# Kernel tuning notes

Measured on AMD Instinct MI355X. Metric: run time of the kernel, lower is better.

The kernel has to match this reference:

```python
import jax, jax.numpy as jnp
import numpy as np

N = 50000   # nodes
E = 800000  # edges
H = 3       # attention heads
IN_F = 128
HID = 128
NUM_CLASSES = 6
GAT_SLOPE = 0.2   # DGL GATConv internal leaky_relu slope
ACT_SLOPE = 0.01  # nn.LeakyReLU default


def setup_inputs() -> dict:
    key = jax.random.key(0)
    ks = jax.random.split(key, 24)
    s = 0.05
    inp = {
        "in_feat": jax.random.normal(ks[0], (N, IN_F), jnp.float32),
        "src": jax.random.randint(ks[1], (E,), 0, N, jnp.int32),
        "dst": jax.random.randint(ks[2], (E,), 0, N, jnp.int32),
        # GATConv 1: W (IN_F, H*HID), attn vectors (H, HID), bias (H*HID)
        "W1": jax.random.normal(ks[3], (IN_F, H * HID), jnp.float32) * s,
        "al1": jax.random.normal(ks[4], (H, HID), jnp.float32) * s,
        "ar1": jax.random.normal(ks[5], (H, HID), jnp.float32) * s,
        "b1": jnp.zeros((H * HID,), jnp.float32),
        # GATConv 2
        "W2": jax.random.normal(ks[6], (HID, H * HID), jnp.float32) * s,
        "al2": jax.random.normal(ks[7], (H, HID), jnp.float32) * s,
        "ar2": jax.random.normal(ks[8], (H, HID), jnp.float32) * s,
        "b2": jnp.zeros((H * HID,), jnp.float32),
    }
    # Dense MLP head lin1..lin4 (HID->HID) and lin5 (HID->NUM_CLASSES)
    for i in range(1, 5):
        inp[f"lw{i}"] = jax.random.normal(ks[8 + 2 * i], (HID, HID), jnp.float32) * s
        inp[f"lb{i}"] = jnp.zeros((HID,), jnp.float32)
    inp["lw5"] = jax.random.normal(ks[20], (HID, NUM_CLASSES), jnp.float32) * s
    inp["lb5"] = jnp.zeros((NUM_CLASSES,), jnp.float32)
    return inp


def gat_conv(x, src, dst, W, al, ar, b):
    # x: (N, F_in) -> out: (N, H, HID)
    h = (x @ W).reshape(N, H, HID)
    el = jnp.einsum('nhf,hf->nh', h, al)  # (N, H)
    er = jnp.einsum('nhf,hf->nh', h, ar)
    e = jax.nn.leaky_relu(el[src] + er[dst], GAT_SLOPE)  # (E, H)
    # edge softmax over incoming edges of each dst node
    m = jax.ops.segment_max(e, dst, num_segments=N)
    m = jnp.where(jnp.isfinite(m), m, 0.0)
    ex = jnp.exp(e - m[dst])
    denom = jax.ops.segment_sum(ex, dst, num_segments=N)
    alpha = ex / (denom[dst] + 1e-9)  # (E, H)
    out = jax.ops.segment_sum(alpha[:, :, None] * h[src], dst, num_segments=N)
    return out + b.reshape(1, H, HID)


def reference(in_feat, src, dst, W1, al1, ar1, b1, W2, al2, ar2, b2,
              lw1, lb1, lw2, lb2, lw3, lb3, lw4, lb4, lw5, lb5):
    act = lambda x: jax.nn.leaky_relu(x, ACT_SLOPE)
    h = act(gat_conv(in_feat, src, dst, W1, al1, ar1, b1)).mean(axis=1)
    h = act(gat_conv(h, src, dst, W2, al2, ar2, b2)).mean(axis=1)
    h = act(h @ lw1 + lb1)
    h = act(h @ lw2 + lb2)
    h = act(h @ lw3 + lb3)
    h = act(h @ lw4 + lb4)
    return h @ lw5 + lb5
```

## Files before the change

### kernel.cpp

```cpp
#include <hip/hip_runtime.h>
#include <hip/hip_bf16.h>


typedef __attribute__((ext_vector_type(8))) short short8;
typedef __attribute__((ext_vector_type(4))) float float4v;
typedef __attribute__((ext_vector_type(2))) float floatx2;

__device__ inline short f2bf(float x) {
    union { float f; unsigned u; } v; v.f = x;
    unsigned r = v.u + 0x7FFFu + ((v.u >> 16) & 1u);
    return (short)(r >> 16);
}
__device__ inline float bf2f(short b) {
    union { float f; unsigned u; } v;
    v.u = ((unsigned)(unsigned short)b) << 16;
    return v.f;
}
__device__ inline short8 zero8() { short8 z = {0,0,0,0,0,0,0,0}; return z; }

#if __has_builtin(__builtin_amdgcn_cvt_pk_fp8_f32)
__device__ inline unsigned short pk2fp8(float a, float b) {
    return (unsigned short)(__builtin_amdgcn_cvt_pk_fp8_f32(a, b, 0, false) & 0xFFFF);
}
#else
__device__ inline unsigned char f2fp8_1(float x) {
    union { float f; unsigned u; } v; v.f = x;
    unsigned s = (v.u >> 24) & 0x80u;
    unsigned au = v.u & 0x7FFFFFFFu;
    if (au >= 0x43E00000u) return (unsigned char)(s | 0x7E);
    if (au < 0x3C800000u) {
        union { float f; unsigned u; } a; a.u = au;
        int k = (int)(a.f * 512.0f + 0.5f);
        if (k > 7) return (unsigned char)(s | 0x08);
        return (unsigned char)(s | (unsigned)k);
    }
    unsigned r = au + 0x0007FFFFu + ((au >> 20) & 1u);
    unsigned e = (r >> 23) - 120u;
    unsigned m = (r >> 20) & 7u;
    if (e >= 15u && m >= 7u) { e = 15u; m = 6u; }
    return (unsigned char)(s | (e << 3) | m);
}
__device__ inline unsigned short pk2fp8(float a, float b) {
    return (unsigned short)f2fp8_1(a) | ((unsigned short)f2fp8_1(b) << 8);
}
#endif

#if __has_builtin(__builtin_amdgcn_cvt_pk_f32_fp8)
__device__ inline floatx2 unpk2fp8(unsigned short p) {
    return __builtin_amdgcn_cvt_pk_f32_fp8((int)p, false);
}
#else
__device__ inline float fp8_1_2f(unsigned char b) {
    unsigned s = b >> 7, e = (b >> 3) & 15u, m = b & 7u;
    float v = (e == 0) ? (float)m * 0.001953125f
                       : (float)(8u + m) * exp2f((float)((int)e - 10));
    return s ? -v : v;
}
__device__ inline floatx2 unpk2fp8(unsigned short p) {
    floatx2 r; r.x = fp8_1_2f((unsigned char)(p & 0xFF));
    r.y = fp8_1_2f((unsigned char)(p >> 8)); return r;
}
#endif

__device__ __forceinline__ void gl_lds16(const short* g, short* l) {
    __builtin_amdgcn_global_load_lds(
        (const __attribute__((address_space(1))) void*)g,
        (__attribute__((address_space(3))) void*)l,
        16, 0, 0);
}

#define SW(r) ((((r) >> 2) ^ (r)) & 3)

#define BM 128
#define BN 128
#define BK 32
#define MSTR 136
#define MROWS 64

__global__ void prep_kernel(
    const float* __restrict__ in_feat, short* __restrict__ P1h,
    short* __restrict__ P1l, int n4, int cb, int wb,
    const int* __restrict__ dst, int* __restrict__ cnt, int E,
    const float* __restrict__ w1, const float* __restrict__ w2,
    const float* __restrict__ m1, const float* __restrict__ m2,
    const float* __restrict__ m3, const float* __restrict__ m4,
    const float* __restrict__ w5,
    short* __restrict__ w1h, short* __restrict__ w1l,
    short* __restrict__ w2h, short* __restrict__ w2l,
    short* __restrict__ m1h, short* __restrict__ m1l,
    short* __restrict__ m2h, short* __restrict__ m2l,
    short* __restrict__ m3h, short* __restrict__ m3l,
    short* __restrict__ m4h, short* __restrict__ m4l,
    short* __restrict__ w5h, short* __restrict__ w5l)
{
    int blk = blockIdx.x;
    if (blk < cb) {
        int i = blk * 256 + threadIdx.x;
        if (i >= n4) return;
        float4 v = *(const float4*)(in_feat + (size_t)i * 4);
        float xs[4] = {v.x, v.y, v.z, v.w};
        short hs[4], ls[4];
        #pragma unroll
        for (int j = 0; j < 4; ++j) {
            hs[j] = f2bf(xs[j]);
            ls[j] = f2bf(xs[j] - bf2f(hs[j]));
        }
        *(uint2*)(P1h + (size_t)i * 4) = *(uint2*)hs;
        *(uint2*)(P1l + (size_t)i * 4) = *(uint2*)ls;
    } else if (blk < cb + wb) {
        int j = (blk - cb) * 256 + threadIdx.x;
        const float* src; short* th; short* tl; int Nc, base;
        if      (j < 49152)  { src = w1; th = w1h; tl = w1l; Nc = 384; base = 0; }
        else if (j < 98304)  { src = w2; th = w2h; tl = w2l; Nc = 384; base = 49152; }
        else if (j < 114688) { src = m1; th = m1h; tl = m1l; Nc = 128; base = 98304; }
        else if (j < 131072) { src = m2; th = m2h; tl = m2l; Nc = 128; base = 114688; }
        else if (j < 147456) { src = m3; th = m3h; tl = m3l; Nc = 128; base = 131072; }
        else if (j < 163840) { src = m4; th = m4h; tl = m4l; Nc = 128; base = 147456; }
        else if (j < 164608) { src = w5; th = w5h; tl = w5l; Nc = 6;   base = 163840; }
        else return;
        int i = j - base;
        int k = i / Nc, c = i - k * Nc;
        float v = src[i];
        short h = f2bf(v);
        th[(size_t)c * 128 + k] = h;
        tl[(size_t)c * 128 + k] = f2bf(v - bf2f(h));
    } else {
        int e = (blk - cb - wb) * 256 + threadIdx.x;
        if (e < E) atomicAdd(&cnt[dst[e]], 1);
    }
}

__global__ __launch_bounds__(256) void gemm_mfma(
    const short* __restrict__ Ahi, const short* __restrict__ Alo,
    const short* __restrict__ Bth, const short* __restrict__ Btl,
    const float* __restrict__ bias,
    float* __restrict__ Cf, short* __restrict__ Chi, short* __restrict__ Clo,
    unsigned char* __restrict__ Cf8,
    float* __restrict__ el, float* __restrict__ er,
    const float* __restrict__ al, const float* __restrict__ ar,
    int M, int Nc, int flags)
{
    __shared__ short Ah[BM * BK], Al_[BM * BK];
    __shared__ short Bh[BN * BK], Bl_[BN * BK];

    int tid = threadIdx.x, lane = tid & 63, wave = tid >> 6;
    int l15 = lane & 15, q = lane >> 4;
    int rowBase = blockIdx.y * BM, colBase = blockIdx.x * BN;

    float4v acc[2][8];
    #pragma unroll
    for (int mt = 0; mt < 2; ++mt)
        #pragma unroll
        for (int nt = 0; nt < 8; ++nt)
            acc[mt][nt] = (float4v){0.f, 0.f, 0.f, 0.f};

    for (int k0 = 0; k0 < 128; k0 += BK) {
        #pragma unroll
        for (int i = 0; i < 2; ++i) {
            int cid = tid + i * 256;
            int r = cid >> 2, sub = cid & 3;
            int gs = (sub ^ SW(r)) * 8;
            size_t ga = (size_t)(rowBase + r) * 128 + k0 + gs;
            size_t gb = (size_t)(colBase + r) * 128 + k0 + gs;
            int ld = cid * 8;
            gl_lds16(Ahi + ga, Ah  + ld);
            gl_lds16(Alo + ga, Al_ + ld);
            gl_lds16(Bth + gb, Bh  + ld);
            gl_lds16(Btl + gb, Bl_ + ld);
        }
        __syncthreads();

        short8 aH[2], aL2[2];
        #pragma unroll
        for (int mt = 0; mt < 2; ++mt) {
            int row = wave * 32 + mt * 16 + l15;
            int off = row * 32 + (q ^ SW(row)) * 8;
            aH[mt]  = *(short8*)&Ah[off];
            aL2[mt] = *(short8*)&Al_[off];
        }
        #pragma unroll
        for (int nt = 0; nt < 8; ++nt) {
            int row = nt * 16 + l15;
            int off = row * 32 + (q ^ SW(row)) * 8;
            short8 bH = *(short8*)&Bh[off];
            short8 bL = *(short8*)&Bl_[off];
            #pragma unroll
            for (int mt = 0; mt < 2; ++mt) {
                acc[mt][nt] = __builtin_amdgcn_mfma_f32_16x16x32_bf16(aH[mt], bH, acc[mt][nt], 0, 0, 0);
                acc[mt][nt] = __builtin_amdgcn_mfma_f32_16x16x32_bf16(aH[mt], bL, acc[mt][nt], 0, 0, 0);
                acc[mt][nt] = __builtin_amdgcn_mfma_f32_16x16x32_bf16(aL2[mt], bH, acc[mt][nt], 0, 0, 0);
            }
        }
        __syncthreads();
    }

    if (flags & 4) {
        const float* alh = al + colBase;
        const float* arh = ar + colBase;
        float pel[2][4] = {}, per_[2][4] = {};
        #pragma unroll
        for (int nt = 0; nt < 8; ++nt) {
            float av = alh[nt * 16 + l15];
            float rv = arh[nt * 16 + l15];
            #pragma unroll
            for (int mt = 0; mt < 2; ++mt)
                #pragma unroll
                for (int i = 0; i < 4; ++i) {
                    pel[mt][i]  += acc[mt][nt][i] * av;
                    per_[mt][i] += acc[mt][nt][i] * rv;
                }
        }
        #pragma unroll
        for (int mask = 1; mask < 16; mask <<= 1)
            #pragma unroll
            for (int mt = 0; mt < 2; ++mt)
                #pragma unroll
                for (int i = 0; i < 4; ++i) {
                    pel[mt][i]  += __shfl_xor(pel[mt][i], mask);
                    per_[mt][i] += __shfl_xor(per_[mt][i], mask);
                }
        if (l15 == 0) {
            #pragma unroll
            for (int mt = 0; mt < 2; ++mt)
                #pragma unroll
                for (int i = 0; i < 4; ++i) {
                    int r = rowBase + wave * 32 + mt * 16 + q * 4 + i;
                    if (r < M) {
                        el[r * 3 + blockIdx.x] = pel[mt][i];
                        er[r * 3 + blockIdx.x] = per_[mt][i];
                    }
                }
        }
    }

    #pragma unroll
    for (int mt = 0; mt < 2; ++mt) {
        #pragma unroll
        for (int nt = 0; nt < 8; ++nt) {
            int c = colBase + nt * 16 + l15;
            bool cok = c < Nc;
            float bv = ((flags & 1) && cok) ? bias[c] : 0.f;
            #pragma unroll
            for (int i = 0; i < 4; ++i) {
                int r = rowBase + wave * 32 + mt * 16 + q * 4 + i;
                float v = acc[mt][nt][i] + bv;
                if (flags & 2) v = (v < 0.f) ? 0.01f * v : v;
                float vn = __shfl_xor(v, 1);
                if (cok && r < M) {
                    size_t idx = (size_t)r * Nc + c;
                    if (flags & 8)  Cf[idx] = v;
                    if (flags & 16) {
                        short hh = f2bf(v);
                        Chi[idx] = hh;
                        if (flags & 32) Clo[idx] = f2bf(v - bf2f(hh));
                    }
                    if ((flags & 64) && !(l15 & 1))
                        *(unsigned short*)(Cf8 + idx) = pk2fp8(v, vn);
                }
            }
        }
    }
}

__global__ __launch_bounds__(256) void mlp_fused(
    const short* __restrict__ Ph, const short* __restrict__ Pl,
    const short* __restrict__ w1h, const short* __restrict__ w1l,
    const short* __restrict__ w2h, const short* __restrict__ w2l,
    const short* __restrict__ w3h, const short* __restrict__ w3l,
    const short* __restrict__ w4h, const short* __restrict__ w4l,
    const short* __restrict__ w5h, const short* __restrict__ w5l,
    const float* __restrict__ b1, const float* __restrict__ b2,
    const float* __restrict__ b3, const float* __restrict__ b4,
    const float* __restrict__ b5,
    float* __restrict__ out, int M)
{
    __shared__ short AH[MROWS * MSTR], AL[MROWS * MSTR];
    __shared__ short WH[128 * BK], WL[128 * BK];

    int tid = threadIdx.x, lane = tid & 63, wave = tid >> 6;
    int l15 = lane & 15, q = lane >> 4;
    int rowBase = blockIdx.x * MROWS;

    #pragma unroll
    for (int s = 0; s < 4; ++s) {
        int idx = tid + s * 256;
        int r = idx >> 4, kq = (idx & 15) * 8;
        int gr = rowBase + r;
        short8 vh = zero8(), vl = zero8();
        if (gr < M) {
            vh = *(const short8*)(Ph + (size_t)gr * 128 + kq);
            vl = *(const short8*)(Pl + (size_t)gr * 128 + kq);
        }
        *(short8*)&AH[r * MSTR + kq] = vh;
        *(short8*)&AL[r * MSTR + kq] = vl;
    }

    const short* Whs[4] = {w1h, w2h, w3h, w4h};
    const short* Wls[4] = {w1l, w2l, w3l, w4l};
    const float* Bss[4] = {b1, b2, b3, b4};

    #pragma unroll
    for (int L = 0; L < 4; ++L) {
        float4v acc[8];
        #pragma unroll
        for (int nt = 0; nt < 8; ++nt)
            acc[nt] = (float4v){0.f, 0.f, 0.f, 0.f};

        for (int k0 = 0; k0 < 128; k0 += BK) {
            #pragma unroll
            for (int i = 0; i < 4; ++i) {
                int c2 = tid + (i & 1) * 256;
                int r = c2 >> 2, sub = c2 & 3;
                int gs = (sub ^ SW(r)) * 8;
                if (i < 2) gl_lds16(Whs[L] + (size_t)r * 128 + k0 + gs, WH + c2 * 8);
                else       gl_lds16(Wls[L] + (size_t)r * 128 + k0 + gs, WL + c2 * 8);
            }
            __syncthreads();
            int offa = (wave * 16 + l15) * MSTR + k0 + q * 8;
            short8 aH  = *(short8*)&AH[offa];
            short8 aL2 = *(short8*)&AL[offa];
            #pragma unroll
            for (int nt = 0; nt < 8; ++nt) {
                int row = nt * 16 + l15;
                int off = row * 32 + (q ^ SW(row)) * 8;
                short8 bH = *(short8*)&WH[off];
                short8 bL = *(short8*)&WL[off];
                acc[nt] = __builtin_amdgcn_mfma_f32_16x16x32_bf16(aH, bH, acc[nt], 0, 0, 0);
                acc[nt] = __builtin_amdgcn_mfma_f32_16x16x32_bf16(aH, bL, acc[nt], 0, 0, 0);
                acc[nt] = __builtin_amdgcn_mfma_f32_16x16x32_bf16(aL2, bH, acc[nt], 0, 0, 0);
            }
            __syncthreads();
        }
        #pragma unroll
        for (int nt = 0; nt < 8; ++nt) {
            int c = nt * 16 + l15;
            float bv = Bss[L][c];
            #pragma unroll
            for (int i = 0; i < 4; ++i) {
                int r = wave * 16 + q * 4 + i;
                float v = acc[nt][i] + bv;
                v = (v < 0.f) ? 0.01f * v : v;
                short hh = f2bf(v);
                AH[r * MSTR + c] = hh;
                AL[r * MSTR + c] = f2bf(v - bf2f(hh));
            }
        }
        __syncthreads();
    }

    float4v acc5 = (float4v){0.f, 0.f, 0.f, 0.f};
    for (int k0 = 0; k0 < 128; k0 += BK) {
        if (tid < 128) {
            int plane = tid >> 6, rem = tid & 63;
            int c = rem >> 2, sub = rem & 3;
            short8 v = zero8();
            if (c < 6)
                v = *(const short8*)((plane ? w5l : w5h) + (size_t)c * 128 + k0 + sub * 8);
            *(short8*)&((plane ? WL : WH)[c * 32 + (sub ^ SW(c)) * 8]) = v;
        }
        __syncthreads();
        int offa = (wave * 16 + l15) * MSTR + k0 + q * 8;
        short8 aH  = *(short8*)&AH[offa];
        short8 aL2 = *(short8*)&AL[offa];
        int offb = l15 * 32 + (q ^ SW(l15)) * 8;
        short8 bH = *(short8*)&WH[offb];
        short8 bL = *(short8*)&WL[offb];
        acc5 = __builtin_amdgcn_mfma_f32_16x16x32_bf16(aH, bH, acc5, 0, 0, 0);
        acc5 = __builtin_amdgcn_mfma_f32_16x16x32_bf16(aH, bL, acc5, 0, 0, 0);
        acc5 = __builtin_amdgcn_mfma_f32_16x16x32_bf16(aL2, bH, acc5, 0, 0, 0);
        __syncthreads();
    }
    if (l15 < 6) {
        float bv = b5[l15];
        #pragma unroll
        for (int i = 0; i < 4; ++i) {
            int r = rowBase + wave * 16 + q * 4 + i;
            if (r < M) out[(size_t)r * 6 + l15] = acc5[i] + bv;
        }
    }
}

__global__ __launch_bounds__(1024) void scan_block(const int* __restrict__ cnt,
                                                   int* __restrict__ off,
                                                   int* __restrict__ bsum, int n)
{
    __shared__ int tmp[1024];
    int tid = threadIdx.x;
    int i = blockIdx.x * 1024 + tid;
    int v = (i < n) ? cnt[i] : 0;
    tmp[tid] = v;
    __syncthreads();
    for (int s = 1; s < 1024; s <<= 1) {
        int t = (tid >= s) ? tmp[tid - s] : 0;
        __syncthreads();
        tmp[tid] += t;
        __syncthreads();
    }
    if (i < n) off[i] = tmp[tid] - v;
    if (tid == 1023) bsum[blockIdx.x] = tmp[1023];
}

__global__ void scan_add2(int* __restrict__ off, const int* __restrict__ bsum,
                          int n, int nb)
{
    __shared__ int pre[64];
    int tid = threadIdx.x;
    if (tid < 64) {
        int v = (tid < nb) ? bsum[tid] : 0;
        #pragma unroll
        for (int s = 1; s < 64; s <<= 1) {
            int t = __shfl_up(v, s);
            if (tid >= s) v += t;
        }
        pre[tid] = v;
    }
    __syncthreads();
    int i = blockIdx.x * blockDim.x + tid;
    if (i < n) {
        int chunk = i >> 10;
        off[i] += chunk ? pre[chunk - 1] : 0;
    }
    if (i == 0) off[n] = pre[nb - 1];
}

__global__ void scatter_kernel(const int* __restrict__ src, const int* __restrict__ dst,
                               const int* __restrict__ off, int* __restrict__ cnt,
                               int* __restrict__ csrc, int E)
{
    int e = blockIdx.x * blockDim.x + threadIdx.x;
    if (e < E) {
        int d = dst[e];
        int p = atomicSub(&cnt[d], 1) - 1;
        csrc[off[d] + p] = src[e];
    }
}

template <bool FP8>
__global__ __launch_bounds__(384) void agg_kernel(
    const void* __restrict__ hsrc, const float* __restrict__ el,
    const float* __restrict__ er, const int* __restrict__ off,
    const int* __restrict__ csrc, const float* __restrict__ bias,
    short* __restrict__ outH, short* __restrict__ outL, int N)
{
    constexpr int ROWB = FP8 ? 384 : 768;
    constexpr int SEGB = ROWB / 3;

    const unsigned char* hb = (const unsigned char*)hsrc;
    int tid = threadIdx.x;
    int u = tid >> 6;
    int nl = u / 3;
    int head = u - nl * 3;
    int l = tid & 63;
    int n = blockIdx.x * 2 + nl;
    bool active = (n < N);

    __shared__ int   ssrcS[6][64];
    __shared__ float swS[6][64];
    __shared__ float smS[2][384];

    int beg = 0, deg = 0;
    float erv = 0.f;
    if (active) {
        beg = off[n];
        deg = off[n + 1] - beg;
        erv = er[n * 3 + head];
    }

    const unsigned char* hseg = hb + head * SEGB + l * (FP8 ? 2 : 4);
    float ax = 0.f, ay = 0.f, denl = 0.f;

    for (int base = 0; base < deg; base += 64) {
        int cnt = min(64, deg - base);
        int s_l = 0; float w = 0.f;
        if (l < cnt) {
            s_l = csrc[beg + base + l];
            float t = el[s_l * 3 + head] + erv;
            t = (t < 0.f) ? 0.2f * t : t;
            w = __expf(t);
        }
        denl += w;
        ssrcS[u][l] = s_l;
        swS[u][l]   = w;
        for (int q0 = 0; q0 < cnt; q0 += 8) {
            int sA[8]; float wA[8]; unsigned vA[8];
            #pragma unroll
            for (int b = 0; b < 8; ++b) {
                int e = q0 + b;
                sA[b] = ssrcS[u][e];
                wA[b] = swS[u][e];
            }
            #pragma unroll
            for (int b = 0; b < 8; ++b) {
                if constexpr (FP8)
                    vA[b] = *(const unsigned short*)(hseg + (size_t)sA[b] * ROWB);
                else
                    vA[b] = *(const unsigned*)(hseg + (size_t)sA[b] * ROWB);
            }
            #pragma unroll
            for (int b = 0; b < 8; ++b) {
                if constexpr (FP8) {
                    floatx2 f = unpk2fp8((unsigned short)vA[b]);
                    ax += wA[b] * f.x;
                    ay += wA[b] * f.y;
                } else {
                    union { unsigned u; float f; } f0, f1;
                    f0.u = vA[b] << 16; f1.u = vA[b] & 0xffff0000u;
                    ax += wA[b] * f0.f;
                    ay += wA[b] * f1.f;
                }
            }
        }
    }

    float den = denl;
    #pragma unroll
    for (int msk = 1; msk < 64; msk <<= 1) den += __shfl_xor(den, msk);
    float r = 1.f / (den + 1e-9f);
    if (deg == 0) r = 0.f;

    if (active) {
        int fb = head * 128 + 2 * l;
        float2 bv = *(const float2*)(bias + fb);
        float vx = ax * r + bv.x; vx = (vx < 0.f) ? 0.01f * vx : vx;
        float vy = ay * r + bv.y; vy = (vy < 0.f) ? 0.01f * vy : vy;
        smS[nl][fb]     = vx;
        smS[nl][fb + 1] = vy;
    }
    __syncthreads();
    if (tid < 128) {
        int mn = tid >> 6;
        int n2 = blockIdx.x * 2 + mn;
        if (n2 < N) {
            int f0i = (tid & 63) * 2, f1i = f0i + 1;
            float mx = (smS[mn][f0i] + smS[mn][128 + f0i] + smS[mn][256 + f0i]) * (1.0f / 3.0f);
            float my = (smS[mn][f1i] + smS[mn][128 + f1i] + smS[mn][256 + f1i]) * (1.0f / 3.0f);
            short hx = f2bf(mx), lx = f2bf(mx - bf2f(hx));
            short hy = f2bf(my), ly = f2bf(my - bf2f(hy));
            unsigned ph = (unsigned)(unsigned short)hx | ((unsigned)(unsigned short)hy << 16);
            unsigned pl = (unsigned)(unsigned short)lx | ((unsigned)(unsigned short)ly << 16);
            *(unsigned*)(outH + (size_t)n2 * 128 + f0i) = ph;
            *(unsigned*)(outL + (size_t)n2 * 128 + f0i) = pl;
        }
    }
}

extern "C" void kernel_launch(void* const* d_in, const int* in_sizes, int n_in,
                              void* d_out, int out_size, void* d_ws, size_t ws_size,
                              hipStream_t stream)
{
    const float* in_feat = (const float*)d_in[0];
    const int*   src     = (const int*)d_in[1];
    const int*   dst     = (const int*)d_in[2];
    const float* W1  = (const float*)d_in[3];
    const float* al1 = (const float*)d_in[4];
    const float* ar1 = (const float*)d_in[5];
    const float* b1  = (const float*)d_in[6];
    const float* W2  = (const float*)d_in[7];
    const float* al2 = (const float*)d_in[8];
    const float* ar2 = (const float*)d_in[9];
    const float* b2  = (const float*)d_in[10];
    const float* lw1 = (const float*)d_in[11];
    const float* lb1 = (const float*)d_in[12];
    const float* lw2 = (const float*)d_in[13];
    const float* lb2 = (const float*)d_in[14];
    const float* lw3 = (const float*)d_in[15];
    const float* lb3 = (const float*)d_in[16];
    const float* lw4 = (const float*)d_in[17];
    const float* lb4 = (const float*)d_in[18];
    const float* lw5 = (const float*)d_in[19];
    const float* lb5 = (const float*)d_in[20];

    const int N = in_sizes[0] / 128;
    const int E = in_sizes[1];

    size_t o = 0;
    auto alloc = [&](size_t bytes) { size_t p = o; o = (o + bytes + 255) & ~(size_t)255; return p; };
    char* ws = (char*)d_ws;
    short* P1h = (short*)(ws + alloc((size_t)N * 128 * 2));
    short* P1l = (short*)(ws + alloc((size_t)N * 128 * 2));
    short* P2h = (short*)(ws + alloc((size_t)N * 128 * 2));
    short* P2l = (short*)(ws + alloc((size_t)N * 128 * 2));
    short* AbH = (short*)(ws + alloc((size_t)N * 384 * 2));
    unsigned char* Af8 = (unsigned char*)(ws + alloc((size_t)N * 384));
    float* el  = (float*)(ws + alloc((size_t)N * 3 * 4));
    float* er  = (float*)(ws + alloc((size_t)N * 3 * 4));
    int*   cnt  = (int*)(ws + alloc((size_t)N * 4));
    int*   off  = (int*)(ws + alloc((size_t)(N + 1) * 4));
    int*   bsum = (int*)(ws + alloc((size_t)4096));
    int*   csrc = (int*)(ws + alloc((size_t)E * 4));
    short* w1th = (short*)(ws + alloc((size_t)384 * 128 * 2));
    short* w1tl = (short*)(ws + alloc((size_t)384 * 128 * 2));
    short* w2th = (short*)(ws + alloc((size_t)384 * 128 * 2));
    short* w2tl = (short*)(ws + alloc((size_t)384 * 128 * 2));
    short* l1th = (short*)(ws + alloc((size_t)128 * 128 * 2));
    short* l1tl = (short*)(ws + alloc((size_t)128 * 128 * 2));
    short* l2th = (short*)(ws + alloc((size_t)128 * 128 * 2));
    short* l2tl = (short*)(ws + alloc((size_t)128 * 128 * 2));
    short* l3th = (short*)(ws + alloc((size_t)128 * 128 * 2));
    short* l3tl = (short*)(ws + alloc((size_t)128 * 128 * 2));
    short* l4th = (short*)(ws + alloc((size_t)128 * 128 * 2));
    short* l4tl = (short*)(ws + alloc((size_t)128 * 128 * 2));
    short* l5th = (short*)(ws + alloc((size_t)6 * 128 * 2));
    short* l5tl = (short*)(ws + alloc((size_t)6 * 128 * 2));
    (void)ws_size;

    float* out = (float*)d_out;

    hipMemsetAsync(cnt, 0, (size_t)N * 4, stream);
    int n4 = N * 128 / 4;
    int cb = (n4 + 255) / 256;
    int wb = (164608 + 255) / 256;
    int hb = (E + 255) / 256;
    prep_kernel<<<cb + wb + hb, 256, 0, stream>>>(
        in_feat, P1h, P1l, n4, cb, wb, dst, cnt, E,
        W1, W2, lw1, lw2, lw3, lw4, lw5,
        w1th, w1tl, w2th, w2tl, l1th, l1tl, l2th, l2tl,
        l3th, l3tl, l4th, l4tl, l5th, l5tl);

    int nb = (N + 1023) / 1024;
    scan_block<<<nb, 1024, 0, stream>>>(cnt, off, bsum, N);
    scan_add2<<<(N + 255) / 256, 256, 0, stream>>>(off, bsum, N, nb);
    scatter_kernel<<<(E + 255) / 256, 256, 0, stream>>>(src, dst, off, cnt, csrc, E);

    int RB = (N + BM - 1) / BM;
    auto gemm = [&](const short* ah, const short* alo, const short* bth, const short* btl,
                    const float* bias, float* cf, short* chi, short* clo,
                    unsigned char* cf8,
                    float* elp, float* erp, const float* alp, const float* arp,
                    int Nc, int flags) {
        dim3 grid((Nc + BN - 1) / BN, RB);
        gemm_mfma<<<grid, 256, 0, stream>>>(ah, alo, bth, btl, bias, cf, chi, clo, cf8,
                                            elp, erp, alp, arp, N, Nc, flags);
    };

    int AGB = (N + 1) / 2;
    gemm(P1h, P1l, w1th, w1tl, nullptr, nullptr, nullptr, nullptr, Af8, el, er, al1, ar1, 384, 4 | 64);
    agg_kernel<true><<<AGB, 384, 0, stream>>>(Af8, el, er, off, csrc, b1, P2h, P2l, N);

    gemm(P2h, P2l, w2th, w2tl, nullptr, nullptr, AbH, nullptr, nullptr, el, er, al2, ar2, 384, 4 | 16);
    agg_kernel<false><<<AGB, 384, 0, stream>>>(AbH, el, er, off, csrc, b2, P1h, P1l, N);

    int RBM = (N + MROWS - 1) / MROWS;
    mlp_fused<<<RBM, 256, 0, stream>>>(P1h, P1l,
                                       l1th, l1tl, l2th, l2tl, l3th, l3tl,
                                       l4th, l4tl, l5th, l5tl,
                                       lb1, lb2, lb3, lb4, lb5, out, N);
}
```

Measured before the change: 520.7 us.

## Quantize projected features to per-row int8 with scale folded into attention weights

Both GAT projections now emit int8 features with a per-row, per-head absmax scale, replacing FP8 for layer 1 and bf16 for layer 2. The scale is stored next to el, so the aggregation loads both as one float2 and folds the scale into the edge weight. This halves the gather bytes for layer 2 and replaces the FP8 unpack with integer-to-float conversion. In exchange the gemm epilogue does an extra max-reduction per row, and int8 quantization of the layer-2 features may lose accuracy compared with bf16.

```diff
diff --git a/kernel.cpp b/kernel.cpp
--- a/kernel.cpp
+++ b/kernel.cpp
@@ -4,7 +4,6 @@
 
 typedef __attribute__((ext_vector_type(8))) short short8;
 typedef __attribute__((ext_vector_type(4))) float float4v;
-typedef __attribute__((ext_vector_type(2))) float floatx2;
 
 __device__ inline short f2bf(float x) {
     union { float f; unsigned u; } v; v.f = x;
@@ -17,50 +16,6 @@
     return v.f;
 }
 __device__ inline short8 zero8() { short8 z = {0,0,0,0,0,0,0,0}; return z; }
-
-#if __has_builtin(__builtin_amdgcn_cvt_pk_fp8_f32)
-__device__ inline unsigned short pk2fp8(float a, float b) {
-    return (unsigned short)(__builtin_amdgcn_cvt_pk_fp8_f32(a, b, 0, false) & 0xFFFF);
-}
-#else
-__device__ inline unsigned char f2fp8_1(float x) {
-    union { float f; unsigned u; } v; v.f = x;
-    unsigned s = (v.u >> 24) & 0x80u;
-    unsigned au = v.u & 0x7FFFFFFFu;
-    if (au >= 0x43E00000u) return (unsigned char)(s | 0x7E);
-    if (au < 0x3C800000u) {
-        union { float f; unsigned u; } a; a.u = au;
-        int k = (int)(a.f * 512.0f + 0.5f);
-        if (k > 7) return (unsigned char)(s | 0x08);
-        return (unsigned char)(s | (unsigned)k);
-    }
-    unsigned r = au + 0x0007FFFFu + ((au >> 20) & 1u);
-    unsigned e = (r >> 23) - 120u;
-    unsigned m = (r >> 20) & 7u;
-    if (e >= 15u && m >= 7u) { e = 15u; m = 6u; }
-    return (unsigned char)(s | (e << 3) | m);
-}
-__device__ inline unsigned short pk2fp8(float a, float b) {
-    return (unsigned short)f2fp8_1(a) | ((unsigned short)f2fp8_1(b) << 8);
-}
-#endif
-
-#if __has_builtin(__builtin_amdgcn_cvt_pk_f32_fp8)
-__device__ inline floatx2 unpk2fp8(unsigned short p) {
-    return __builtin_amdgcn_cvt_pk_f32_fp8((int)p, false);
-}
-#else
-__device__ inline float fp8_1_2f(unsigned char b) {
-    unsigned s = b >> 7, e = (b >> 3) & 15u, m = b & 7u;
-    float v = (e == 0) ? (float)m * 0.001953125f
-                       : (float)(8u + m) * exp2f((float)((int)e - 10));
-    return s ? -v : v;
-}
-__device__ inline floatx2 unpk2fp8(unsigned short p) {
-    floatx2 r; r.x = fp8_1_2f((unsigned char)(p & 0xFF));
-    r.y = fp8_1_2f((unsigned char)(p >> 8)); return r;
-}
-#endif
 
 __device__ __forceinline__ void gl_lds16(const short* g, short* l) {
     __builtin_amdgcn_global_load_lds(
@@ -133,12 +88,10 @@
 __global__ __launch_bounds__(256) void gemm_mfma(
     const short* __restrict__ Ahi, const short* __restrict__ Alo,
     const short* __restrict__ Bth, const short* __restrict__ Btl,
-    const float* __restrict__ bias,
-    float* __restrict__ Cf, short* __restrict__ Chi, short* __restrict__ Clo,
-    unsigned char* __restrict__ Cf8,
-    float* __restrict__ el, float* __restrict__ er,
+    unsigned char* __restrict__ Cq,
+    float* __restrict__ els, float* __restrict__ er,
     const float* __restrict__ al, const float* __restrict__ ar,
-    int M, int Nc, int flags)
+    int M, int Nc)
 {
     __shared__ short Ah[BM * BK], Al_[BM * BK];
     __shared__ short Bh[BN * BK], Bl_[BN * BK];
@@ -194,7 +147,7 @@
         __syncthreads();
     }
 
-    if (flags & 4) {
+    {
         const float* alh = al + colBase;
         const float* arh = ar + colBase;
         float pel[2][4] = {}, per_[2][4] = {};
@@ -226,7 +179,7 @@
                 for (int i = 0; i < 4; ++i) {
                     int r = rowBase + wave * 32 + mt * 16 + q * 4 + i;
                     if (r < M) {
-                        el[r * 3 + blockIdx.x] = pel[mt][i];
+                        els[(size_t)(r * 3 + blockIdx.x) * 2] = pel[mt][i];
                         er[r * 3 + blockIdx.x] = per_[mt][i];
                     }
                 }
@@ -236,26 +189,26 @@
     #pragma unroll
     for (int mt = 0; mt < 2; ++mt) {
         #pragma unroll
-        for (int nt = 0; nt < 8; ++nt) {
-            int c = colBase + nt * 16 + l15;
-            bool cok = c < Nc;
-            float bv = ((flags & 1) && cok) ? bias[c] : 0.f;
-            #pragma unroll
-            for (int i = 0; i < 4; ++i) {
-                int r = rowBase + wave * 32 + mt * 16 + q * 4 + i;
-                float v = acc[mt][nt][i] + bv;
-                if (flags & 2) v = (v < 0.f) ? 0.01f * v : v;
-                float vn = __shfl_xor(v, 1);
-                if (cok && r < M) {
-                    size_t idx = (size_t)r * Nc + c;
-                    if (flags & 8)  Cf[idx] = v;
-                    if (flags & 16) {
-                        short hh = f2bf(v);
-                        Chi[idx] = hh;
-                        if (flags & 32) Clo[idx] = f2bf(v - bf2f(hh));
-                    }
-                    if ((flags & 64) && !(l15 & 1))
-                        *(unsigned short*)(Cf8 + idx) = pk2fp8(v, vn);
+        for (int i = 0; i < 4; ++i) {
+            float rm = 0.f;
+            #pragma unroll
+            for (int nt = 0; nt < 8; ++nt)
+                rm = fmaxf(rm, fabsf(acc[mt][nt][i]));
+            #pragma unroll
+            for (int mask = 1; mask < 16; mask <<= 1)
+                rm = fmaxf(rm, __shfl_xor(rm, mask));
+            int r = rowBase + wave * 32 + mt * 16 + q * 4 + i;
+            float inv = 127.f / fmaxf(rm, 1e-30f);
+            if (l15 == 0 && r < M)
+                els[(size_t)(r * 3 + blockIdx.x) * 2 + 1] = rm * (1.f / 127.f);
+            #pragma unroll
+            for (int nt = 0; nt < 8; ++nt) {
+                int c = colBase + nt * 16 + l15;
+                int qi = (int)rintf(acc[mt][nt][i] * inv);
+                int qn = __shfl_xor(qi, 1);
+                if (!(l15 & 1) && r < M && c < Nc) {
+                    unsigned short pk = (unsigned short)((qi & 0xFF) | ((qn & 0xFF) << 8));
+                    *(unsigned short*)(Cq + (size_t)r * Nc + c) = pk;
                 }
             }
         }
@@ -435,17 +388,12 @@
     }
 }
 
-template <bool FP8>
 __global__ __launch_bounds__(384) void agg_kernel(
-    const void* __restrict__ hsrc, const float* __restrict__ el,
+    const unsigned char* __restrict__ h8, const float* __restrict__ els,
     const float* __restrict__ er, const int* __restrict__ off,
     const int* __restrict__ csrc, const float* __restrict__ bias,
     short* __restrict__ outH, short* __restrict__ outL, int N)
 {
-    constexpr int ROWB = FP8 ? 384 : 768;
-    constexpr int SEGB = ROWB / 3;
-
-    const unsigned char* hb = (const unsigned char*)hsrc;
     int tid = threadIdx.x;
     int u = tid >> 6;
     int nl = u / 3;
@@ -466,21 +414,23 @@
         erv = er[n * 3 + head];
     }
 
-    const unsigned char* hseg = hb + head * SEGB + l * (FP8 ? 2 : 4);
+    const unsigned char* hseg = h8 + head * 128 + l * 2;
     float ax = 0.f, ay = 0.f, denl = 0.f;
 
     for (int base = 0; base < deg; base += 64) {
         int cnt = min(64, deg - base);
-        int s_l = 0; float w = 0.f;
+        int s_l = 0; float w = 0.f, wS = 0.f;
         if (l < cnt) {
             s_l = csrc[beg + base + l];
-            float t = el[s_l * 3 + head] + erv;
+            float2 e2 = *(const float2*)(els + (size_t)(s_l * 3 + head) * 2);
+            float t = e2.x + erv;
             t = (t < 0.f) ? 0.2f * t : t;
             w = __expf(t);
+            wS = w * e2.y;
         }
         denl += w;
         ssrcS[u][l] = s_l;
-        swS[u][l]   = w;
+        swS[u][l]   = wS;
         for (int q0 = 0; q0 < cnt; q0 += 8) {
             int sA[8]; float wA[8]; unsigned vA[8];
             #pragma unroll
@@ -490,24 +440,14 @@
                 wA[b] = swS[u][e];
             }
             #pragma unroll
+            for (int b = 0; b < 8; ++b)
+                vA[b] = *(const unsigned short*)(hseg + (size_t)sA[b] * 384);
+            #pragma unroll
             for (int b = 0; b < 8; ++b) {
-                if constexpr (FP8)
-                    vA[b] = *(const unsigned short*)(hseg + (size_t)sA[b] * ROWB);
-                else
-                    vA[b] = *(const unsigned*)(hseg + (size_t)sA[b] * ROWB);
-            }
-            #pragma unroll
-            for (int b = 0; b < 8; ++b) {
-                if constexpr (FP8) {
-                    floatx2 f = unpk2fp8((unsigned short)vA[b]);
-                    ax += wA[b] * f.x;
-                    ay += wA[b] * f.y;
-                } else {
-                    union { unsigned u; float f; } f0, f1;
-                    f0.u = vA[b] << 16; f1.u = vA[b] & 0xffff0000u;
-                    ax += wA[b] * f0.f;
-                    ay += wA[b] * f1.f;
-                }
+                int b0 = (int)(signed char)(vA[b] & 0xFF);
+                int b1 = (int)(signed char)((vA[b] >> 8) & 0xFF);
+                ax += wA[b] * (float)b0;
+                ay += wA[b] * (float)b1;
             }
         }
     }
@@ -580,9 +520,8 @@
     short* P1l = (short*)(ws + alloc((size_t)N * 128 * 2));
     short* P2h = (short*)(ws + alloc((size_t)N * 128 * 2));
     short* P2l = (short*)(ws + alloc((size_t)N * 128 * 2));
-    short* AbH = (short*)(ws + alloc((size_t)N * 384 * 2));
-    unsigned char* Af8 = (unsigned char*)(ws + alloc((size_t)N * 384));
-    float* el  = (float*)(ws + alloc((size_t)N * 3 * 4));
+    unsigned char* Aq = (unsigned char*)(ws + alloc((size_t)N * 384));
+    float* els = (float*)(ws + alloc((size_t)N * 3 * 2 * 4));
     float* er  = (float*)(ws + alloc((size_t)N * 3 * 4));
     int*   cnt  = (int*)(ws + alloc((size_t)N * 4));
     int*   off  = (int*)(ws + alloc((size_t)(N + 1) * 4));
@@ -623,22 +562,16 @@
     scatter_kernel<<<(E + 255) / 256, 256, 0, stream>>>(src, dst, off, cnt, csrc, E);
 
     int RB = (N + BM - 1) / BM;
-    auto gemm = [&](const short* ah, const short* alo, const short* bth, const short* btl,
-                    const float* bias, float* cf, short* chi, short* clo,
-                    unsigned char* cf8,
-                    float* elp, float* erp, const float* alp, const float* arp,
-                    int Nc, int flags) {
-        dim3 grid((Nc + BN - 1) / BN, RB);
-        gemm_mfma<<<grid, 256, 0, stream>>>(ah, alo, bth, btl, bias, cf, chi, clo, cf8,
-                                            elp, erp, alp, arp, N, Nc, flags);
-    };
-
+    dim3 ggrid(3, RB);
     int AGB = (N + 1) / 2;
-    gemm(P1h, P1l, w1th, w1tl, nullptr, nullptr, nullptr, nullptr, Af8, el, er, al1, ar1, 384, 4 | 64);
-    agg_kernel<true><<<AGB, 384, 0, stream>>>(Af8, el, er, off, csrc, b1, P2h, P2l, N);
-
-    gemm(P2h, P2l, w2th, w2tl, nullptr, nullptr, AbH, nullptr, nullptr, el, er, al2, ar2, 384, 4 | 16);
-    agg_kernel<false><<<AGB, 384, 0, stream>>>(AbH, el, er, off, csrc, b2, P1h, P1l, N);
+
+    gemm_mfma<<<ggrid, 256, 0, stream>>>(P1h, P1l, w1th, w1tl, Aq, els, er,
+                                         al1, ar1, N, 384);
+    agg_kernel<<<AGB, 384, 0, stream>>>(Aq, els, er, off, csrc, b1, P2h, P2l, N);
+
+    gemm_mfma<<<ggrid, 256, 0, stream>>>(P2h, P2l, w2th, w2tl, Aq, els, er,
+                                         al2, ar2, N, 384);
+    agg_kernel<<<AGB, 384, 0, stream>>>(Aq, els, er, off, csrc, b2, P1h, P1l, N);
 
     int RBM = (N + MROWS - 1) / MROWS;
     mlp_fused<<<RBM, 256, 0, stream>>>(P1h, P1l,
```

Result: faster. 495.7 us (-4.8%).
